# Performance work log

Measured on AMD Instinct MI355X. Metric: run time of the kernel, lower is better.

Reference implementation:

```python
import jax, jax.numpy as jnp
import numpy as np

N = 524288   # total spokes
D = 128      # dim_hidden
B = 128      # graphs in batch
H = 64       # hubs per graph (static, num_hubs_type='S')
K = 4        # hubs_per_spoke


def setup_inputs() -> dict:
    key = jax.random.key(0)
    ks = jax.random.split(key, 5)
    x = jax.random.normal(ks[0], (N, D), jnp.float32)
    spoke_init_hub_idx = jax.random.randint(ks[1], (N,), 0, H)
    batch_idx = jnp.sort(jax.random.randint(ks[2], (N,), 0, B))
    s1 = 1.0 / np.sqrt(D)
    s2 = 1.0 / np.sqrt(2 * D)
    W1 = jax.random.uniform(ks[3], (D, 2 * D), jnp.float32, -s1, s1)
    b1 = jnp.zeros((2 * D,), jnp.float32)
    W2 = jax.random.uniform(ks[4], (2 * D, D), jnp.float32, -s2, s2)
    b2 = jnp.zeros((D,), jnp.float32)
    return {"x": x, "spoke_init_hub_idx": spoke_init_hub_idx, "batch_idx": batch_idx,
            "W1": W1, "b1": b1, "W2": W2, "b2": b2}


def reference(x, spoke_init_hub_idx, batch_idx, W1, b1, W2, b2):
    # FeedForward on spokes: Linear -> GELU(exact, torch default) -> Linear
    h = jax.nn.gelu(x @ W1 + b1, approximate=False) @ W2 + b2  # [N, D]

    # batched hub index: local hub idx offset by graph (uniform H hubs/graph)
    gidx = batch_idx * H + spoke_init_hub_idx  # [N]

    # scatter_mean of spoke features into hubs (empty hubs -> 0, as torch scatter_mean)
    sums = jax.ops.segment_sum(h, gidx, num_segments=B * H)                    # [B*H, D]
    cnt = jax.ops.segment_sum(jnp.ones((N,), h.dtype), gidx, num_segments=B * H)
    hub_features = sums / jnp.maximum(cnt, 1.0)[:, None]                       # [B*H, D]

    # assign each spoke to the K hubs closest to its initial hub (within its graph)
    hf = hub_features.reshape(B, H, D)
    d2 = jnp.sum((hf[:, :, None, :] - hf[:, None, :, :]) ** 2, axis=-1)        # [B, H, H]
    _, knn = jax.lax.top_k(-d2, K)                                             # [B, H, K] local hub ids
    hubs_idx = knn[batch_idx, spoke_init_hub_idx] + batch_idx[:, None] * H     # [N, K] global hub ids
    spokes_idx = jnp.repeat(jnp.arange(N), K)
    spokes_hubs_edge_index = jnp.stack([spokes_idx, hubs_idx.reshape(-1)], axis=0)  # [2, N*K]

    return hub_features, spokes_hubs_edge_index
```

## Files before the change

kernel.cpp:

```cpp
#include <hip/hip_runtime.h>
#include <hip/hip_bf16.h>

#define N_SPOKES 524288
#define DIM      128
#define DIM2     256
#define NB       128
#define NH       64
#define BH       8192

#define OUT_HF   0
#define OUT_E0   1048576
#define OUT_E1   3145728

typedef __attribute__((ext_vector_type(8))) short  short8;
typedef __attribute__((ext_vector_type(4))) float  float4v;
typedef __attribute__((ext_vector_type(4))) unsigned short ushort4v;

__device__ inline unsigned short f2bf(float f) {
    __hip_bfloat16 h = __float2bfloat16(f);
    return *reinterpret_cast<unsigned short*>(&h);
}

__device__ inline float gelu_f(float v) {
    float s = v * (1.0f + 0.044715f * v * v);
    float e = __builtin_exp2f(-2.302118131f * s);
    return v * __builtin_amdgcn_rcpf(1.0f + e);
}

__global__ void setup_kernel(const int* __restrict__ batchidx, const int* __restrict__ hubidx,
                             const float* __restrict__ W1,
                             unsigned short* __restrict__ w1t,
                             int* __restrict__ goff, int* __restrict__ cnt) {
    int b = blockIdx.x, tid = threadIdx.x;
    if (b < 2048) {
        int i = b * 256 + tid;
        if (i < N_SPOKES) {
            int bi = batchidx[i];
            int bp = (i == 0) ? -1 : batchidx[i - 1];
            for (int g = bp + 1; g <= bi; ++g) goff[g] = i;
            if (i == N_SPOKES - 1)
                for (int g = bi + 1; g <= NB; ++g) goff[g] = N_SPOKES;
            atomicAdd(&cnt[bi * NH + hubidx[i]], 1);
        }
    } else {
        int idx = (b - 2048) * 256 + tid;
        if (idx < DIM * DIM2) {
            int n = idx >> 7, k = idx & 127;
            w1t[idx] = f2bf(W1[k * DIM2 + n]);
        }
    }
}

__launch_bounds__(512, 4)
__global__ void ffn_fused(const float* __restrict__ x,
                          const int* __restrict__ hubidx,
                          const int* __restrict__ goff,
                          const unsigned short* __restrict__ w1t,
                          const float* __restrict__ b1,
                          float* __restrict__ outbuf,
                          int atomic_mode) {
    __shared__ unsigned short sA[128 * 136];
    __shared__ unsigned short sU[256 * 40];
    __shared__ unsigned short sOne[64 * 136];

    const int tid  = threadIdx.x;
    const int lane = tid & 63;
    const int w    = tid >> 6;
    const int c_lo = lane & 15;
    const int c_hi = lane >> 4;
    const int wcb  = w * 32;
    const int g      = blockIdx.x >> 2;
    const int cchunk = blockIdx.x & 3;

    const int s = goff[g], e = goff[g + 1];
    const int len = e - s;
    const int cs  = (len + 3) >> 2;
    const int ms  = s + cchunk * cs;
    int me = ms + cs; if (me > e) me = e;
    const int n  = me - ms;
    const int nt = (n > 0) ? ((n + 127) >> 7) : 0;

    short8 bfr[2][4];
    #pragma unroll
    for (int n4 = 0; n4 < 2; ++n4)
        #pragma unroll
        for (int k = 0; k < 4; ++k) {
            int col = wcb + n4 * 16 + c_lo;
            bfr[n4][k] = *(const short8*)(w1t + col * DIM + k * 32 + c_hi * 8);
        }
    float bcol[2];
    #pragma unroll
    for (int n4 = 0; n4 < 2; ++n4) bcol[n4] = b1[wcb + n4 * 16 + c_lo];

    float4v hacc[4][2];
    #pragma unroll
    for (int mt = 0; mt < 4; ++mt)
        #pragma unroll
        for (int n4 = 0; n4 < 2; ++n4) hacc[mt][n4] = (float4v){0.f, 0.f, 0.f, 0.f};

    for (int i = tid; i < 2048; i += 512)
        *(unsigned long long*)&sOne[(i >> 5) * 136 + (i & 31) * 4] = 0ULL;

    const float4v* x4 = (const float4v*)x;

    float4v pf[8];
    int hub_nxt = -1;
    if (nt > 0) {
        #pragma unroll
        for (int it = 0; it < 8; ++it) {
            int f = it * 512 + tid;
            int r = f >> 5;
            int rr = r < n ? r : n - 1;
            pf[it] = x4[(size_t)(ms + rr) * 32 + (f & 31)];
        }
        if (tid < 128) hub_nxt = (tid < n) ? hubidx[ms + tid] : -1;
    }
    __syncthreads();

    for (int t = 0; t < nt; ++t) {
        const int hub_cur = hub_nxt;
        #pragma unroll
        for (int it = 0; it < 8; ++it) {
            int f = it * 512 + tid;
            int row = f >> 5, c4 = f & 31;
            float4v v = pf[it];
            ushort4v u = { f2bf(v.x), f2bf(v.y), f2bf(v.z), f2bf(v.w) };
            *(ushort4v*)&sA[row * 136 + c4 * 4] = u;
        }
        if (tid < 128 && hub_cur >= 0)
            sOne[hub_cur * 136 + tid] = (unsigned short)0x3F80;
        __syncthreads();

        if (t + 1 < nt) {
            #pragma unroll
            for (int it = 0; it < 8; ++it) {
                int f = it * 512 + tid;
                int r = (t + 1) * 128 + (f >> 5);
                int rr = r < n ? r : n - 1;
                pf[it] = x4[(size_t)(ms + rr) * 32 + (f & 31)];
            }
            if (tid < 128) {
                int r = (t + 1) * 128 + tid;
                hub_nxt = (r < n) ? hubidx[ms + r] : -1;
            }
        }

        #pragma unroll
        for (int ks = 0; ks < 4; ++ks) {
            float4v acc[2][2];
            #pragma unroll
            for (int m2 = 0; m2 < 2; ++m2)
                #pragma unroll
                for (int n4 = 0; n4 < 2; ++n4) acc[m2][n4] = (float4v){0.f, 0.f, 0.f, 0.f};

            #pragma unroll
            for (int k = 0; k < 4; ++k)
                #pragma unroll
                for (int m2 = 0; m2 < 2; ++m2) {
                    short8 a = *(const short8*)&sA[(ks * 32 + m2 * 16 + c_lo) * 136 + k * 32 + c_hi * 8];
                    acc[m2][0] = __builtin_amdgcn_mfma_f32_16x16x32_bf16(a, bfr[0][k], acc[m2][0], 0, 0, 0);
                    acc[m2][1] = __builtin_amdgcn_mfma_f32_16x16x32_bf16(a, bfr[1][k], acc[m2][1], 0, 0, 0);
                }

            #pragma unroll
            for (int m2 = 0; m2 < 2; ++m2) {
                int rbase = m2 * 16 + c_hi * 4;
                #pragma unroll
                for (int n4 = 0; n4 < 2; ++n4) {
                    int col = wcb + n4 * 16 + c_lo;
                    float4v a4 = acc[m2][n4];
                    ushort4v u;
                    u.x = f2bf(gelu_f(a4.x + bcol[n4]));
                    u.y = f2bf(gelu_f(a4.y + bcol[n4]));
                    u.z = f2bf(gelu_f(a4.z + bcol[n4]));
                    u.w = f2bf(gelu_f(a4.w + bcol[n4]));
                    *(ushort4v*)&sU[col * 40 + rbase] = u;
                }
            }

            short8 aS[4];
            #pragma unroll
            for (int mt = 0; mt < 4; ++mt)
                aS[mt] = *(const short8*)&sOne[(mt * 16 + c_lo) * 136 + ks * 32 + c_hi * 8];
            short8 bU[2];
            #pragma unroll
            for (int n4 = 0; n4 < 2; ++n4)
                bU[n4] = *(const short8*)&sU[(wcb + n4 * 16 + c_lo) * 40 + c_hi * 8];
            #pragma unroll
            for (int mt = 0; mt < 4; ++mt)
                #pragma unroll
                for (int n4 = 0; n4 < 2; ++n4)
                    hacc[mt][n4] = __builtin_amdgcn_mfma_f32_16x16x32_bf16(aS[mt], bU[n4], hacc[mt][n4], 0, 0, 0);
        }
        __syncthreads();
        if (tid < 128 && hub_cur >= 0)
            sOne[hub_cur * 136 + tid] = 0;
    }

    #pragma unroll
    for (int mt = 0; mt < 4; ++mt)
        #pragma unroll
        for (int n4 = 0; n4 < 2; ++n4) {
            float4v v = hacc[mt][n4];
            int col = wcb + n4 * 16 + c_lo;
            #pragma unroll
            for (int reg = 0; reg < 4; ++reg) {
                int hub = mt * 16 + c_hi * 4 + reg;
                size_t o = ((size_t)g * NH + hub) * DIM2 + col;
                if (atomic_mode) atomicAdd(&outbuf[o], v[reg]);
                else outbuf[(size_t)cchunk * BH * DIM2 + o] = v[reg];
            }
        }
}

__global__ void hubfeat_kernel(const float* __restrict__ part, int nchunk,
                               const int* __restrict__ cnt,
                               const float* __restrict__ W2, const float* __restrict__ b2,
                               float* __restrict__ out) {
    __shared__ float sSum[16 * 256];
    int tid = threadIdx.x;
    int d   = tid & 127;
    int hh  = tid >> 7;

    for (int i = tid; i < 16 * 256; i += 256) {
        size_t o = (size_t)(blockIdx.x * 16) * DIM2 + i;
        float v = 0.f;
        for (int c = 0; c < nchunk; ++c) v += part[(size_t)c * BH * DIM2 + o];
        sSum[i] = v;
    }
    __syncthreads();

    int h0 = hh * 8;
    float acc[8] = {0.f, 0.f, 0.f, 0.f, 0.f, 0.f, 0.f, 0.f};
    for (int k4 = 0; k4 < 64; ++k4) {
        float w0 = W2[(k4 * 4 + 0) * DIM + d];
        float w1 = W2[(k4 * 4 + 1) * DIM + d];
        float w2 = W2[(k4 * 4 + 2) * DIM + d];
        float w3 = W2[(k4 * 4 + 3) * DIM + d];
        #pragma unroll
        for (int j = 0; j < 8; ++j) {
            float4v sv = *(const float4v*)&sSum[(h0 + j) * 256 + k4 * 4];
            acc[j] += sv.x * w0 + sv.y * w1 + sv.z * w2 + sv.w * w3;
        }
    }
    float b2d = b2[d];
    #pragma unroll
    for (int j = 0; j < 8; ++j) {
        int h = blockIdx.x * 16 + h0 + j;
        float c = (float)cnt[h];
        out[OUT_HF + h * DIM + d] = (acc[j] + c * b2d) / fmaxf(c, 1.0f);
    }
}

__global__ void knn_edges(const float* __restrict__ hf, const int* __restrict__ goff,
                          const int* __restrict__ hubidx, float* __restrict__ out) {
    __shared__ float s[64 * 129];
    __shared__ float d2[64 * 64];
    __shared__ int sK[64 * 4];
    int g = blockIdx.x, tid = threadIdx.x;

    for (int i = tid; i < 64 * 128; i += 256) {
        int r = i >> 7, c = i & 127;
        s[r * 129 + c] = hf[OUT_HF + (g * 64 + r) * DIM + c];
    }
    __syncthreads();

    for (int p = tid; p < 4096; p += 256) {
        int i = p >> 6, j = p & 63;
        float a = 0.f;
        for (int k = 0; k < 128; ++k) {
            float dd = s[i * 129 + k] - s[j * 129 + k];
            a += dd * dd;
        }
        d2[p] = a;
    }
    __syncthreads();

    if (tid < 64) {
        float bv0 = 1e30f, bv1 = 1e30f, bv2 = 1e30f, bv3 = 1e30f;
        int   bi0 = 0,     bi1 = 0,     bi2 = 0,     bi3 = 0;
        for (int j = 0; j < 64; ++j) {
            float v = d2[tid * 64 + j];
            if (v < bv0)      { bv3=bv2; bi3=bi2; bv2=bv1; bi2=bi1; bv1=bv0; bi1=bi0; bv0=v; bi0=j; }
            else if (v < bv1) { bv3=bv2; bi3=bi2; bv2=bv1; bi2=bi1; bv1=v;   bi1=j; }
            else if (v < bv2) { bv3=bv2; bi3=bi2; bv2=v;   bi2=j; }
            else if (v < bv3) { bv3=v;   bi3=j; }
        }
        sK[tid * 4 + 0] = bi0; sK[tid * 4 + 1] = bi1;
        sK[tid * 4 + 2] = bi2; sK[tid * 4 + 3] = bi3;
    }
    __syncthreads();

    int sgs = goff[g], sge = goff[g + 1];
    float gbase = (float)(g * NH);
    for (int i = sgs + tid; i < sge; i += 256) {
        int h = hubidx[i];
        int4 kn = *(const int4*)&sK[h * 4];
        float fi = (float)i;
        float4v o0 = { fi, fi, fi, fi };
        ((float4v*)(out + OUT_E0))[i] = o0;
        float4v o1 = { kn.x + gbase, kn.y + gbase, kn.z + gbase, kn.w + gbase };
        ((float4v*)(out + OUT_E1))[i] = o1;
    }
}

extern "C" void kernel_launch(void* const* d_in, const int* in_sizes, int n_in,
                              void* d_out, int out_size, void* d_ws, size_t ws_size,
                              hipStream_t stream) {
    const float* x        = (const float*)d_in[0];
    const int*   hubidx   = (const int*)d_in[1];
    const int*   batchidx = (const int*)d_in[2];
    const float* W1       = (const float*)d_in[3];
    const float* b1       = (const float*)d_in[4];
    const float* W2       = (const float*)d_in[5];
    const float* b2       = (const float*)d_in[6];
    float* out = (float*)d_out;
    char*  ws  = (char*)d_ws;

    const size_t need_partial = 33654784;
    int atomic_mode = (ws_size < need_partial) ? 1 : 0;

    float*          part;
    int*            cnt;
    unsigned short* w1t;
    int*            goff;
    if (!atomic_mode) {
        part = (float*)ws;
        cnt  = (int*)(ws + 33554432);
        w1t  = (unsigned short*)(ws + 33587200);
        goff = (int*)(ws + 33652736);
    } else {
        part = (float*)ws;
        cnt  = (int*)(ws + 8388608);
        w1t  = (unsigned short*)(ws + 8421376);
        goff = (int*)(ws + 8486912);
    }

    (void)hipMemsetAsync(cnt, 0, 32768, stream);
    if (atomic_mode) (void)hipMemsetAsync(part, 0, 8388608, stream);

    setup_kernel<<<2176, 256, 0, stream>>>(batchidx, hubidx, W1, w1t, goff, cnt);
    ffn_fused   <<<512,  512, 0, stream>>>(x, hubidx, goff, w1t, b1, part, atomic_mode);
    hubfeat_kernel<<<512, 256, 0, stream>>>(part, atomic_mode ? 1 : 4, cnt, W2, b2, out);
    knn_edges   <<<NB,   256, 0, stream>>>(out, goff, hubidx, out);
}
```

Baseline: 554.8 us.

## Drop register prefetch of x tiles and use packed bf16 conversions

Removes the 8-register float4 software prefetch of the next x tile. The current tile is now loaded directly at the top of each iteration, then converted and stored to LDS. Float-to-bf16 conversion for the x tile and the GELU output now uses packed two-element conversions. This frees 32 VGPRs, which may raise occupancy, but global load latency is no longer hidden behind the MFMA work of the previous tile.

```diff
diff --git a/kernel.cpp b/kernel.cpp
--- a/kernel.cpp
+++ b/kernel.cpp
@@ -19,6 +19,13 @@
 __device__ inline unsigned short f2bf(float f) {
     __hip_bfloat16 h = __float2bfloat16(f);
     return *reinterpret_cast<unsigned short*>(&h);
+}
+
+__device__ inline unsigned int pkbf(float a, float b) {
+    __hip_bfloat162 h = __float22bfloat162_rn(make_float2(a, b));
+    union { __hip_bfloat162 h; unsigned int u; } cv;
+    cv.h = h;
+    return cv.u;
 }
 
 __device__ inline float gelu_f(float v) {
@@ -103,46 +110,39 @@
 
     const float4v* x4 = (const float4v*)x;
 
-    float4v pf[8];
     int hub_nxt = -1;
-    if (nt > 0) {
-        #pragma unroll
-        for (int it = 0; it < 8; ++it) {
-            int f = it * 512 + tid;
-            int r = f >> 5;
-            int rr = r < n ? r : n - 1;
-            pf[it] = x4[(size_t)(ms + rr) * 32 + (f & 31)];
-        }
-        if (tid < 128) hub_nxt = (tid < n) ? hubidx[ms + tid] : -1;
-    }
+    if (nt > 0 && tid < 128) hub_nxt = (tid < n) ? hubidx[ms + tid] : -1;
     __syncthreads();
 
     for (int t = 0; t < nt; ++t) {
         const int hub_cur = hub_nxt;
-        #pragma unroll
-        for (int it = 0; it < 8; ++it) {
-            int f = it * 512 + tid;
-            int row = f >> 5, c4 = f & 31;
-            float4v v = pf[it];
-            ushort4v u = { f2bf(v.x), f2bf(v.y), f2bf(v.z), f2bf(v.w) };
-            *(ushort4v*)&sA[row * 136 + c4 * 4] = u;
-        }
-        if (tid < 128 && hub_cur >= 0)
-            sOne[hub_cur * 136 + tid] = (unsigned short)0x3F80;
-        __syncthreads();
-
-        if (t + 1 < nt) {
+
+        {
+            float4v ld[8];
             #pragma unroll
             for (int it = 0; it < 8; ++it) {
                 int f = it * 512 + tid;
-                int r = (t + 1) * 128 + (f >> 5);
+                int r = t * 128 + (f >> 5);
                 int rr = r < n ? r : n - 1;
-                pf[it] = x4[(size_t)(ms + rr) * 32 + (f & 31)];
+                ld[it] = x4[(size_t)(ms + rr) * 32 + (f & 31)];
             }
-            if (tid < 128) {
-                int r = (t + 1) * 128 + tid;
-                hub_nxt = (r < n) ? hubidx[ms + r] : -1;
+            if (tid < 128 && hub_cur >= 0)
+                sOne[hub_cur * 136 + tid] = (unsigned short)0x3F80;
+            #pragma unroll
+            for (int it = 0; it < 8; ++it) {
+                int f = it * 512 + tid;
+                int row = f >> 5, c4 = f & 31;
+                float4v v = ld[it];
+                unsigned int lo = pkbf(v.x, v.y);
+                unsigned int hi = pkbf(v.z, v.w);
+                *(uint2*)&sA[row * 136 + c4 * 4] = make_uint2(lo, hi);
             }
+        }
+        __syncthreads();
+
+        if (t + 1 < nt && tid < 128) {
+            int r = (t + 1) * 128 + tid;
+            hub_nxt = (r < n) ? hubidx[ms + r] : -1;
         }
 
         #pragma unroll
@@ -169,12 +169,9 @@
                 for (int n4 = 0; n4 < 2; ++n4) {
                     int col = wcb + n4 * 16 + c_lo;
                     float4v a4 = acc[m2][n4];
-                    ushort4v u;
-                    u.x = f2bf(gelu_f(a4.x + bcol[n4]));
-                    u.y = f2bf(gelu_f(a4.y + bcol[n4]));
-                    u.z = f2bf(gelu_f(a4.z + bcol[n4]));
-                    u.w = f2bf(gelu_f(a4.w + bcol[n4]));
-                    *(ushort4v*)&sU[col * 40 + rbase] = u;
+                    unsigned int lo = pkbf(gelu_f(a4.x + bcol[n4]), gelu_f(a4.y + bcol[n4]));
+                    unsigned int hi = pkbf(gelu_f(a4.z + bcol[n4]), gelu_f(a4.w + bcol[n4]));
+                    *(uint2*)&sU[col * 40 + rbase] = make_uint2(lo, hi);
                 }
             }
 
```

Result: faster. 516.8 us (-6.8%).
